# Kernel optimization log

Measured on AMD Instinct MI355X. Metric: run time of the kernel, lower is better.

## Reference

```python
import jax, jax.numpy as jnp
import numpy as np

N_NODES = 100000
N_EDGES = 1600000
D_IN = 128
D_OUT = 128
KEEP_PROB = 0.5  # torch code: p_drop = 1 - self.dropout, dropout=0.5


def setup_inputs() -> dict:
    key = jax.random.key(0)
    k1, k2, k3, k4, k5 = jax.random.split(key, 5)
    x = jax.random.normal(k1, (N_NODES, D_IN), dtype=jnp.float32)
    # Glorot uniform init matching weight_variable_glorot
    init_range = np.sqrt(6.0 / (D_IN + D_OUT))
    W = jax.random.uniform(k2, (D_IN, D_OUT), dtype=jnp.float32,
                           minval=-init_range, maxval=init_range)
    adj_row = jax.random.randint(k3, (N_EDGES,), 0, N_NODES, dtype=jnp.int32)
    adj_col = jax.random.randint(k4, (N_EDGES,), 0, N_NODES, dtype=jnp.int32)
    adj_val = jax.random.uniform(k5, (N_EDGES,), dtype=jnp.float32)
    return {"x": x, "W": W, "adj_row": adj_row, "adj_col": adj_col, "adj_val": adj_val}


def reference(x, W, adj_row, adj_col, adj_val):
    # dropout (always training=True in the torch module), deterministic key
    mask = jax.random.bernoulli(jax.random.key(42), KEEP_PROB, x.shape)
    x = jnp.where(mask, x / KEEP_PROB, 0.0)
    # dense GEMM: [N, D_in] @ [D_in, D_out]
    h = x @ W
    # sparse adjacency SpMM in COO form: out[r] += val * h[c]
    msg = adj_val[:, None] * h[adj_col]            # [E, D_out]
    agg = jax.ops.segment_sum(msg, adj_row, num_segments=N_NODES)
    return jax.nn.relu(agg)
```

## Files before the change

### kernel.cpp

```cpp
#include <hip/hip_runtime.h>
#include <hip/hip_bf16.h>

#define N_NODES 100000
#define N_EDGES 1600000
#define D 128
#define NC 391
#define CCAP 5120
#define NF 3125
#define FCAP 640
#define C1S 32

typedef float          floatx4 __attribute__((ext_vector_type(4)));
typedef __bf16         bf16x8  __attribute__((ext_vector_type(8)));
typedef unsigned short ushort8 __attribute__((ext_vector_type(8)));

__device__ __forceinline__ unsigned rotl32(unsigned x, int d) {
    return (x << d) | (x >> (32 - d));
}

__device__ __forceinline__ void threefry_0_42(unsigned c0, unsigned c1,
                                              unsigned& o0, unsigned& o1) {
    const unsigned k0 = 0u, k1 = 42u;
    const unsigned k2 = 0x1BD11BDAu ^ k0 ^ k1;
    unsigned x0 = c0 + k0;
    unsigned x1 = c1 + k1;
#define TF_R4(r0, r1, r2, r3)                      \
    x0 += x1; x1 = rotl32(x1, r0); x1 ^= x0;       \
    x0 += x1; x1 = rotl32(x1, r1); x1 ^= x0;       \
    x0 += x1; x1 = rotl32(x1, r2); x1 ^= x0;       \
    x0 += x1; x1 = rotl32(x1, r3); x1 ^= x0;
    TF_R4(13, 15, 26, 6);  x0 += k1; x1 += k2 + 1u;
    TF_R4(17, 29, 16, 24); x0 += k2; x1 += k0 + 2u;
    TF_R4(13, 15, 26, 6);  x0 += k0; x1 += k1 + 3u;
    TF_R4(17, 29, 16, 24); x0 += k1; x1 += k2 + 4u;
    TF_R4(13, 15, 26, 6);  x0 += k2; x1 += k0 + 5u;
#undef TF_R4
    o0 = x0; o1 = x1;
}

__device__ __forceinline__ bool keep_elem(unsigned i) {
    unsigned o0, o1;
    threefry_0_42(0u, i, o0, o1);
    return (((o0 ^ o1) >> 31) == 0u);
}

__device__ __forceinline__ unsigned short f32_bf16(float f) {
    unsigned u = __float_as_uint(f);
    u += 0x7fffu + ((u >> 16) & 1u);
    return (unsigned short)(u >> 16);
}

__global__ __launch_bounds__(256)
void k_gemm(const float* __restrict__ x, const float* __restrict__ W,
            unsigned short* __restrict__ hb) {
    __shared__ __align__(16) unsigned short Wt[128][136];
    __shared__ __align__(16) unsigned short xs[32][136];

    const int t = threadIdx.x;
    const int g = blockIdx.x;

    {
        int n      = t & 127;
        int k8base = t >> 7;
#pragma unroll
        for (int it = 0; it < 8; ++it) {
            int k8 = (it * 2 + k8base) * 8;
            unsigned short tmp[8];
#pragma unroll
            for (int j = 0; j < 8; ++j)
                tmp[j] = f32_bf16(W[(k8 + j) * 128 + n]);
            *(ushort8*)&Wt[n][k8] = *(ushort8*)tmp;
        }
    }
    {
        int m  = t >> 4;
        int c0 = (t & 15) * 8;
        int r0 = g * 32 + m;
        const float* pa = x + r0 * D + c0;
        const float* pb = x + (r0 + 16) * D + c0;
        float va[8], vb[8];
        *(float4*)&va[0] = ((const float4*)pa)[0];
        *(float4*)&va[4] = ((const float4*)pa)[1];
        *(float4*)&vb[0] = ((const float4*)pb)[0];
        *(float4*)&vb[4] = ((const float4*)pb)[1];
        int ibase = r0 * D + c0;
        unsigned short ta[8], tb[8];
#pragma unroll
        for (int j = 0; j < 8; ++j) {
            float fa = keep_elem((unsigned)(ibase + j))        ? 2.0f * va[j] : 0.0f;
            float fb = keep_elem((unsigned)(ibase + 2048 + j)) ? 2.0f * vb[j] : 0.0f;
            ta[j] = f32_bf16(fa);
            tb[j] = f32_bf16(fb);
        }
        *(ushort8*)&xs[m][c0]      = *(ushort8*)ta;
        *(ushort8*)&xs[16 + m][c0] = *(ushort8*)tb;
    }
    __syncthreads();

    const int w  = t >> 6;
    const int l  = t & 63;
    const int rt = w >> 1;
    const int ctbase = (w & 1) * 4;
    const int mm = l & 15;
    const int q  = l >> 4;
    const int koff = q * 8;
    const unsigned short* xrow = &xs[rt * 16 + mm][0];
    const int growbase = g * 32 + rt * 16;

    for (int ci = 0; ci < 4; ++ci) {
        int ct = ctbase + ci;
        const unsigned short* wrow = &Wt[ct * 16 + mm][0];
        floatx4 acc = {0.f, 0.f, 0.f, 0.f};
#pragma unroll
        for (int kt = 0; kt < 4; ++kt) {
            bf16x8 a = *(const bf16x8*)(xrow + kt * 32 + koff);
            bf16x8 b = *(const bf16x8*)(wrow + kt * 32 + koff);
            acc = __builtin_amdgcn_mfma_f32_16x16x32_bf16(a, b, acc, 0, 0, 0);
        }
        int col = ct * 16 + mm;
#pragma unroll
        for (int reg = 0; reg < 4; ++reg) {
            int grow = growbase + q * 4 + reg;
            hb[grow * D + col] = f32_bf16(acc[reg]);
        }
    }
}

__global__ __launch_bounds__(256)
void k_bucket1(const int* __restrict__ row, const int* __restrict__ col,
               const float* __restrict__ val, int* __restrict__ cnt1,
               int2* __restrict__ buf) {
    __shared__ int h[NC];
    __shared__ int lbase[NC];
    const int t = threadIdx.x;
    for (int i = t; i < NC; i += 256) h[i] = 0;
    __syncthreads();

    int rows[16], cols[16];
    float vals[16];
    int base = blockIdx.x * 4096;
#pragma unroll
    for (int k = 0; k < 4; ++k) {
        int e4 = base + (k * 256 + t) * 4;
        if (e4 < N_EDGES) {
            *(int4*)&rows[k * 4]   = *(const int4*)(row + e4);
            *(int4*)&cols[k * 4]   = *(const int4*)(col + e4);
            *(float4*)&vals[k * 4] = *(const float4*)(val + e4);
        } else {
            rows[k * 4] = rows[k * 4 + 1] = rows[k * 4 + 2] = rows[k * 4 + 3] = -1;
        }
    }
#pragma unroll
    for (int j = 0; j < 16; ++j)
        if (rows[j] >= 0) atomicAdd(&h[rows[j] >> 8], 1);
    __syncthreads();

    for (int i = t; i < NC; i += 256) {
        int c = h[i];
        lbase[i] = c ? atomicAdd(&cnt1[i * C1S], c) : 0;
    }
    __syncthreads();
    for (int i = t; i < NC; i += 256) h[i] = 0;
    __syncthreads();

#pragma unroll
    for (int j = 0; j < 16; ++j) {
        if (rows[j] >= 0) {
            int bb  = rows[j] >> 8;
            int pos = lbase[bb] + atomicAdd(&h[bb], 1);
            if (pos < CCAP) {
                int2 ent;
                ent.x = (cols[j] << 7) | ((rows[j] & 255) << 24);
                ent.y = __float_as_int(vals[j]);
                buf[bb * CCAP + pos] = ent;
            }
        }
    }
}

__global__ __launch_bounds__(512)
void k_split(const int* __restrict__ cnt1, int2* __restrict__ buf,
             int* __restrict__ cnt2) {
    __shared__ int h[8][9];
    __shared__ int cur[8][9];

    const int c = blockIdx.x, t = threadIdx.x, w = t >> 6;
    int n = cnt1[c * C1S];
    if (n > CCAP) n = CCAP;
    int2* slab = buf + c * CCAP;

    if (t < 72) ((int*)h)[t] = 0;
    __syncthreads();

    int2 er[10];
    int  bin[10];
#pragma unroll
    for (int k = 0; k < 10; ++k) {
        int i = k * 512 + t;
        if (i < n) {
            er[k]  = slab[i];
            bin[k] = ((unsigned)er[k].x) >> 29;
            atomicAdd(&h[w][bin[k]], 1);
        } else {
            bin[k] = -1;
        }
    }
    __syncthreads();

    if (t < 8) {
        int s = 0;
#pragma unroll
        for (int wv = 0; wv < 8; ++wv) {
            cur[wv][t] = s;
            s += h[wv][t];
        }
        cnt2[c * 8 + t] = s;
    }
    __syncthreads();
    if (t < 64) {
        int wv = t >> 3, b = t & 7;
        cur[wv][b] += b * FCAP;
    }
    __syncthreads();

#pragma unroll
    for (int k = 0; k < 10; ++k) {
        if (bin[k] >= 0) {
            int pos = atomicAdd(&cur[w][bin[k]], 1);
            if (pos < (bin[k] + 1) * FCAP)
                slab[pos] = er[k];
        }
    }
}

__global__ __launch_bounds__(256, 8)
void k_sortgather(const int* __restrict__ cnt2, const int2* __restrict__ buf,
                  const unsigned short* __restrict__ hb, float* __restrict__ out) {
    __shared__ __align__(16) int2 ents2[FCAP];
    __shared__ int cnt_[32];
    __shared__ int scan_[32];
    __shared__ int cur_[32];

    const int b = blockIdx.x, t = threadIdx.x;
    const int2* slab = buf + (b >> 3) * CCAP + (b & 7) * FCAP;
    int n = cnt2[b];
    if (n > FCAP) n = FCAP;

    if (t < 32) cnt_[t] = 0;
    __syncthreads();

    int2 er[3];
    int  rl_[3];
#pragma unroll
    for (int k = 0; k < 3; ++k) {
        int i = k * 256 + t;
        if (i < n) {
            er[k]  = slab[i];
            rl_[k] = ((unsigned)er[k].x >> 24) & 31;
            atomicAdd(&cnt_[rl_[k]], 1);
        } else {
            rl_[k] = -1;
        }
    }
    __syncthreads();

    if (t < 32) {
        int v = cnt_[t];
        int x = v;
#pragma unroll
        for (int off = 1; off < 32; off <<= 1) {
            int u = __shfl_up(x, off);
            if (t >= off) x += u;
        }
        scan_[t] = x;
        cur_[t]  = x - v;
    }
    __syncthreads();

#pragma unroll
    for (int k = 0; k < 3; ++k) {
        if (rl_[k] >= 0) {
            int pos = atomicAdd(&cur_[rl_[k]], 1);
            ents2[pos] = er[k];
        }
    }
    __syncthreads();

    const int w  = t >> 6;
    const int l2 = (t & 63) * 2;
    const unsigned short* hbl = hb + l2;
    for (int r = 0; r < 8; ++r) {
        int rl = w * 8 + r;
        int c  = cnt_[rl];
        int b0 = scan_[rl] - c;
        float a0 = 0.f, a1 = 0.f;
        int i = 0;
        for (; i + 16 <= c; i += 16) {
            unsigned ex[16];
            float    vv[16];
#pragma unroll
            for (int j = 0; j < 16; ++j) {
                int2 e = ents2[b0 + i + j];
                ex[j] = (unsigned)e.x & 0xFFFFFFu;
                vv[j] = __int_as_float(e.y);
            }
            unsigned hv[16];
#pragma unroll
            for (int j = 0; j < 16; ++j)
                hv[j] = *(const unsigned*)(hbl + ex[j]);
#pragma unroll
            for (int j = 0; j < 16; ++j) {
                a0 = fmaf(vv[j], __uint_as_float(hv[j] << 16), a0);
                a1 = fmaf(vv[j], __uint_as_float(hv[j] & 0xffff0000u), a1);
            }
        }
        for (; i + 4 <= c; i += 4) {
            unsigned ex[4];
            float    vv[4];
#pragma unroll
            for (int j = 0; j < 4; ++j) {
                int2 e = ents2[b0 + i + j];
                ex[j] = (unsigned)e.x & 0xFFFFFFu;
                vv[j] = __int_as_float(e.y);
            }
            unsigned hv[4];
#pragma unroll
            for (int j = 0; j < 4; ++j)
                hv[j] = *(const unsigned*)(hbl + ex[j]);
#pragma unroll
            for (int j = 0; j < 4; ++j) {
                a0 = fmaf(vv[j], __uint_as_float(hv[j] << 16), a0);
                a1 = fmaf(vv[j], __uint_as_float(hv[j] & 0xffff0000u), a1);
            }
        }
        for (; i < c; ++i) {
            int2 e = ents2[b0 + i];
            float v = __int_as_float(e.y);
            unsigned hv = *(const unsigned*)(hbl + ((unsigned)e.x & 0xFFFFFFu));
            a0 = fmaf(v, __uint_as_float(hv << 16), a0);
            a1 = fmaf(v, __uint_as_float(hv & 0xffff0000u), a1);
        }
        int grow = (b << 5) + rl;
        float2 rr;
        rr.x = a0 > 0.f ? a0 : 0.f;
        rr.y = a1 > 0.f ? a1 : 0.f;
        *(float2*)(out + grow * D + l2) = rr;
    }
}

extern "C" void kernel_launch(void* const* d_in, const int* in_sizes, int n_in,
                              void* d_out, int out_size, void* d_ws, size_t ws_size,
                              hipStream_t stream) {
    const float* x    = (const float*)d_in[0];
    const float* W    = (const float*)d_in[1];
    const int*   arow = (const int*)d_in[2];
    const int*   acol = (const int*)d_in[3];
    const float* aval = (const float*)d_in[4];
    float* out = (float*)d_out;

    char* ws = (char*)d_ws;
    unsigned short* hb = (unsigned short*)ws;
    size_t off = 25600000;
    int* cnt1 = (int*)(ws + off); off += NC * C1S * 4;
    off = (off + 127) & ~(size_t)127;
    int* cnt2 = (int*)(ws + off); off += 3136 * 4;
    off = (off + 127) & ~(size_t)127;
    int2* buf = (int2*)(ws + off); off += (size_t)NC * CCAP * 8;

    hipMemsetAsync(cnt1, 0, NC * C1S * 4, stream);
    k_bucket1    <<<NC, 256, 0, stream>>>(arow, acol, aval, cnt1, buf);
    k_split      <<<NC, 512, 0, stream>>>(cnt1, buf, cnt2);
    k_gemm       <<<3125, 256, 0, stream>>>(x, W, hb);
    k_sortgather <<<NF, 256, 0, stream>>>(cnt2, buf, hb, out);
}
```

Before: 229.4 us.

## Co-schedule GEMM halves with bucketing kernels and fully sort rows per chunk

```diff
diff --git a/kernel.cpp b/kernel.cpp
--- a/kernel.cpp
+++ b/kernel.cpp
@@ -7,8 +7,11 @@
 #define NC 391
 #define CCAP 5120
 #define NF 3125
-#define FCAP 640
 #define C1S 32
+#define RSS 257
+#define GCAP 1024
+#define GEMM_H1 1563
+#define GEMM_H2 1562
 
 typedef float          floatx4 __attribute__((ext_vector_type(4)));
 typedef __bf16         bf16x8  __attribute__((ext_vector_type(8)));
@@ -50,15 +53,12 @@
     return (unsigned short)(u >> 16);
 }
 
-__global__ __launch_bounds__(256)
-void k_gemm(const float* __restrict__ x, const float* __restrict__ W,
-            unsigned short* __restrict__ hb) {
-    __shared__ __align__(16) unsigned short Wt[128][136];
-    __shared__ __align__(16) unsigned short xs[32][136];
-
-    const int t = threadIdx.x;
-    const int g = blockIdx.x;
-
+__device__ __forceinline__ void gemm_body(const float* __restrict__ x,
+                                          const float* __restrict__ W,
+                                          unsigned short* __restrict__ hb,
+                                          unsigned short (*Wt)[136],
+                                          unsigned short (*xs)[136],
+                                          int g, int t) {
     {
         int n      = t & 127;
         int k8base = t >> 7;
@@ -127,12 +127,22 @@
 }
 
 __global__ __launch_bounds__(256)
-void k_bucket1(const int* __restrict__ row, const int* __restrict__ col,
-               const float* __restrict__ val, int* __restrict__ cnt1,
-               int2* __restrict__ buf) {
+void k_p1(const float* __restrict__ x, const float* __restrict__ W,
+          unsigned short* __restrict__ hb,
+          const int* __restrict__ row, const int* __restrict__ col,
+          const float* __restrict__ val, int* __restrict__ cnt1,
+          int2* __restrict__ buf) {
+    __shared__ __align__(16) unsigned short Wt[128][136];
+    __shared__ __align__(16) unsigned short xs[32][136];
     __shared__ int h[NC];
     __shared__ int lbase[NC];
+
     const int t = threadIdx.x;
+    if (blockIdx.x >= NC) {
+        gemm_body(x, W, hb, Wt, xs, blockIdx.x - NC, t);
+        return;
+    }
+
     for (int i = t; i < NC; i += 256) h[i] = 0;
     __syncthreads();
 
@@ -178,112 +188,89 @@
     }
 }
 
-__global__ __launch_bounds__(512)
-void k_split(const int* __restrict__ cnt1, int2* __restrict__ buf,
-             int* __restrict__ cnt2) {
-    __shared__ int h[8][9];
-    __shared__ int cur[8][9];
-
-    const int c = blockIdx.x, t = threadIdx.x, w = t >> 6;
+__global__ __launch_bounds__(256)
+void k_p2(const float* __restrict__ x, const float* __restrict__ W,
+          unsigned short* __restrict__ hb,
+          const int* __restrict__ cnt1, int2* __restrict__ buf,
+          int* __restrict__ rs) {
+    __shared__ __align__(16) unsigned short Wt[128][136];
+    __shared__ __align__(16) unsigned short xs[32][136];
+    __shared__ int h[4][256];
+    __shared__ int wsum[4];
+
+    const int t = threadIdx.x;
+    if (blockIdx.x >= NC) {
+        gemm_body(x, W, hb, Wt, xs, blockIdx.x - NC + GEMM_H1, t);
+        return;
+    }
+
+    const int c = blockIdx.x;
+    const int w = t >> 6;
     int n = cnt1[c * C1S];
     if (n > CCAP) n = CCAP;
     int2* slab = buf + c * CCAP;
 
-    if (t < 72) ((int*)h)[t] = 0;
-    __syncthreads();
-
-    int2 er[10];
-    int  bin[10];
-#pragma unroll
-    for (int k = 0; k < 10; ++k) {
-        int i = k * 512 + t;
-        if (i < n) {
-            er[k]  = slab[i];
-            bin[k] = ((unsigned)er[k].x) >> 29;
-            atomicAdd(&h[w][bin[k]], 1);
-        } else {
-            bin[k] = -1;
-        }
-    }
-    __syncthreads();
-
-    if (t < 8) {
-        int s = 0;
-#pragma unroll
-        for (int wv = 0; wv < 8; ++wv) {
-            cur[wv][t] = s;
-            s += h[wv][t];
-        }
-        cnt2[c * 8 + t] = s;
-    }
-    __syncthreads();
-    if (t < 64) {
-        int wv = t >> 3, b = t & 7;
-        cur[wv][b] += b * FCAP;
-    }
-    __syncthreads();
-
-#pragma unroll
-    for (int k = 0; k < 10; ++k) {
-        if (bin[k] >= 0) {
-            int pos = atomicAdd(&cur[w][bin[k]], 1);
-            if (pos < (bin[k] + 1) * FCAP)
-                slab[pos] = er[k];
-        }
-    }
-}
-
-__global__ __launch_bounds__(256, 8)
-void k_sortgather(const int* __restrict__ cnt2, const int2* __restrict__ buf,
-                  const unsigned short* __restrict__ hb, float* __restrict__ out) {
-    __shared__ __align__(16) int2 ents2[FCAP];
-    __shared__ int cnt_[32];
-    __shared__ int scan_[32];
-    __shared__ int cur_[32];
-
-    const int b = blockIdx.x, t = threadIdx.x;
-    const int2* slab = buf + (b >> 3) * CCAP + (b & 7) * FCAP;
-    int n = cnt2[b];
-    if (n > FCAP) n = FCAP;
-
-    if (t < 32) cnt_[t] = 0;
-    __syncthreads();
-
-    int2 er[3];
-    int  rl_[3];
-#pragma unroll
-    for (int k = 0; k < 3; ++k) {
+    for (int i = t; i < 1024; i += 256) ((int*)h)[i] = 0;
+    __syncthreads();
+
+    int2 er[20];
+#pragma unroll
+    for (int k = 0; k < 20; ++k) {
         int i = k * 256 + t;
         if (i < n) {
-            er[k]  = slab[i];
-            rl_[k] = ((unsigned)er[k].x >> 24) & 31;
-            atomicAdd(&cnt_[rl_[k]], 1);
-        } else {
-            rl_[k] = -1;
-        }
-    }
-    __syncthreads();
-
-    if (t < 32) {
-        int v = cnt_[t];
-        int x = v;
-#pragma unroll
-        for (int off = 1; off < 32; off <<= 1) {
-            int u = __shfl_up(x, off);
-            if (t >= off) x += u;
-        }
-        scan_[t] = x;
-        cur_[t]  = x - v;
-    }
-    __syncthreads();
-
-#pragma unroll
-    for (int k = 0; k < 3; ++k) {
-        if (rl_[k] >= 0) {
-            int pos = atomicAdd(&cur_[rl_[k]], 1);
-            ents2[pos] = er[k];
-        }
-    }
+            er[k] = slab[i];
+            atomicAdd(&h[w][((unsigned)er[k].x) >> 24], 1);
+        }
+    }
+    __syncthreads();
+
+    int v = h[0][t] + h[1][t] + h[2][t] + h[3][t];
+    int xsc = v;
+#pragma unroll
+    for (int off = 1; off < 64; off <<= 1) {
+        int u = __shfl_up(xsc, off);
+        if ((t & 63) >= off) xsc += u;
+    }
+    if ((t & 63) == 63) wsum[t >> 6] = xsc;
+    __syncthreads();
+    int wo = 0;
+    for (int k = 0; k < (t >> 6); ++k) wo += wsum[k];
+    int basex = xsc - v + wo;
+    rs[c * RSS + t] = basex;
+    if (t == 0) rs[c * RSS + 256] = n;
+    int s = basex;
+#pragma unroll
+    for (int wv = 0; wv < 4; ++wv) {
+        int tmp = h[wv][t];
+        h[wv][t] = s;
+        s += tmp;
+    }
+    __syncthreads();
+
+#pragma unroll
+    for (int k = 0; k < 20; ++k) {
+        int i = k * 256 + t;
+        if (i < n) {
+            int pos = atomicAdd(&h[w][((unsigned)er[k].x) >> 24], 1);
+            slab[pos] = er[k];
+        }
+    }
+}
+
+__global__ __launch_bounds__(256, 8)
+void k_gather(const int* __restrict__ rs, const int2* __restrict__ buf,
+              const unsigned short* __restrict__ hb, float* __restrict__ out) {
+    __shared__ __align__(16) int2 eL[GCAP];
+
+    const int b = blockIdx.x, t = threadIdx.x;
+    const int c = b >> 3;
+    const int2* slab = buf + c * CCAP;
+    const int* rsb = rs + c * RSS + (b & 7) * 32;
+    const int rs0 = rsb[0];
+    int nf = rsb[32] - rs0;
+    if (nf > GCAP) nf = GCAP;
+
+    for (int i = t; i < nf; i += 256) eL[i] = slab[rs0 + i];
     __syncthreads();
 
     const int w  = t >> 6;
@@ -291,16 +278,18 @@
     const unsigned short* hbl = hb + l2;
     for (int r = 0; r < 8; ++r) {
         int rl = w * 8 + r;
-        int c  = cnt_[rl];
-        int b0 = scan_[rl] - c;
+        int s0 = rsb[rl] - rs0;
+        int e0 = rsb[rl + 1] - rs0;
+        if (e0 > nf) e0 = nf;
+        int cc = e0 - s0;
         float a0 = 0.f, a1 = 0.f;
         int i = 0;
-        for (; i + 16 <= c; i += 16) {
+        for (; i + 16 <= cc; i += 16) {
             unsigned ex[16];
             float    vv[16];
 #pragma unroll
             for (int j = 0; j < 16; ++j) {
-                int2 e = ents2[b0 + i + j];
+                int2 e = eL[s0 + i + j];
                 ex[j] = (unsigned)e.x & 0xFFFFFFu;
                 vv[j] = __int_as_float(e.y);
             }
@@ -314,12 +303,12 @@
                 a1 = fmaf(vv[j], __uint_as_float(hv[j] & 0xffff0000u), a1);
             }
         }
-        for (; i + 4 <= c; i += 4) {
+        for (; i + 4 <= cc; i += 4) {
             unsigned ex[4];
             float    vv[4];
 #pragma unroll
             for (int j = 0; j < 4; ++j) {
-                int2 e = ents2[b0 + i + j];
+                int2 e = eL[s0 + i + j];
                 ex[j] = (unsigned)e.x & 0xFFFFFFu;
                 vv[j] = __int_as_float(e.y);
             }
@@ -333,8 +322,8 @@
                 a1 = fmaf(vv[j], __uint_as_float(hv[j] & 0xffff0000u), a1);
             }
         }
-        for (; i < c; ++i) {
-            int2 e = ents2[b0 + i];
+        for (; i < cc; ++i) {
+            int2 e = eL[s0 + i];
             float v = __int_as_float(e.y);
             unsigned hv = *(const unsigned*)(hbl + ((unsigned)e.x & 0xFFFFFFu));
             a0 = fmaf(v, __uint_as_float(hv << 16), a0);
@@ -363,13 +352,12 @@
     size_t off = 25600000;
     int* cnt1 = (int*)(ws + off); off += NC * C1S * 4;
     off = (off + 127) & ~(size_t)127;
-    int* cnt2 = (int*)(ws + off); off += 3136 * 4;
+    int* rs   = (int*)(ws + off); off += NC * RSS * 4;
     off = (off + 127) & ~(size_t)127;
     int2* buf = (int2*)(ws + off); off += (size_t)NC * CCAP * 8;
 
     hipMemsetAsync(cnt1, 0, NC * C1S * 4, stream);
-    k_bucket1    <<<NC, 256, 0, stream>>>(arow, acol, aval, cnt1, buf);
-    k_split      <<<NC, 512, 0, stream>>>(cnt1, buf, cnt2);
-    k_gemm       <<<3125, 256, 0, stream>>>(x, W, hb);
-    k_sortgather <<<NF, 256, 0, stream>>>(cnt2, buf, hb, out);
-}
+    k_p1     <<<NC + GEMM_H1, 256, 0, stream>>>(x, W, hb, arow, acol, aval, cnt1, buf);
+    k_p2     <<<NC + GEMM_H2, 256, 0, stream>>>(x, W, hb, cnt1, buf, rs);
+    k_gather <<<NF, 256, 0, stream>>>(rs, buf, hb, out);
+}
```

Result: faster. 222.5 us (-3.0%).
